# Optimization experiments

Measured on AMD Instinct MI355X. Metric: run time of the kernel, lower is better.

Reference implementation:

```python
import jax, jax.numpy as jnp
import numpy as np

_EPS = 1e-8

def setup_inputs() -> dict:
    key = jax.random.key(0)
    k1, k2, k3, k4 = jax.random.split(key, 4)
    L, B, H, S = 12, 8, 12, 384
    M, NL, NH = 32, 3, 4
    attn = jax.random.uniform(k1, (L, B, H, S, S), dtype=jnp.float32)
    references = jax.random.uniform(k2, (M, S, S), dtype=jnp.float32)
    layer_idx = jax.random.randint(k3, (M, NL), 0, L)
    head_idx = jax.random.randint(k4, (M, NH), 0, H)
    return {"attn": attn, "references": references,
            "layer_idx": layer_idx, "head_idx": head_idx}

def reference(attn, references, layer_idx, head_idx):
    # attn: [L,B,H,S,S] stacked attention maps; references: [M,S,S]
    L, B, H, S, _ = attn.shape
    M, nl = layer_idx.shape
    nh = head_idx.shape[1]
    rows = jnp.arange(M)[:, None]
    # One-hot averaging matrices: patch mean over selected layers/heads.
    # .add handles repeated indices the same way the gather-then-mean does.
    Wl = jnp.zeros((M, L), attn.dtype).at[rows, layer_idx].add(1.0 / nl)
    Wh = jnp.zeros((M, H), attn.dtype).at[rows, head_idx].add(1.0 / nh)
    # patch_means[m,b,s,t] = mean over patch layers/heads of attn
    patch_means = jnp.einsum('ml,mh,lbhst->mbst', Wl, Wh, attn)  # [M,B,S,S]
    flat = patch_means.reshape(M, B, S * S)
    ref = references.reshape(M, 1, S * S)
    # torch .std is unbiased (ddof=1) over the batch axis
    std = jnp.maximum(jnp.std(flat, axis=1, ddof=1, keepdims=True), _EPS)
    z = (flat - ref) / std
    scores = jnp.mean(z * z, axis=-1)  # [M,B]
    return scores.T  # [B,M]
```

## Files before the change

kernel.cpp:

```cpp
#include <hip/hip_runtime.h>

#define L_DIM 12
#define B_DIM 8
#define H_DIM 12
#define S_DIM 384
#define S2    (S_DIM * S_DIM)
#define M_DIM 32
#define NL 3
#define NH 4
#define CH 512
#define NCH (S2 / CH)
#define NXCD 8

template <bool ATOMIC>
__global__ __launch_bounds__(128) void pfe_main(
    const float* __restrict__ attn,
    const float* __restrict__ refs,
    const int*   __restrict__ lidx,
    const int*   __restrict__ hidx,
    float*       __restrict__ outp)
{
    const int p    = blockIdx.x;
    const int xcd  = p & (NXCD - 1);
    const int slot = p >> 3;
    const int m    = slot & (M_DIM - 1);
    const int lc   = slot >> 5;
    const int chunk = lc * NXCD + xcd;
    const int tid  = threadIdx.x;
    const unsigned st = (unsigned)chunk * CH + (unsigned)tid * 4;

    __shared__ int   s_mk[NL * NH];
    __shared__ float s_mw[NL * NH];
    __shared__ int   s_nm;
    __shared__ float s_red[2 * B_DIM];

    if (tid == 0) {
        int keys[NL * NH];
#pragma unroll
        for (int i = 0; i < NL; ++i) {
            const int l = lidx[m * NL + i];
#pragma unroll
            for (int j = 0; j < NH; ++j)
                keys[i * NH + j] = l * 16 + hidx[m * NH + j];
        }
        for (int i = 1; i < NL * NH; ++i) {
            const int k = keys[i];
            int j = i - 1;
            for (; j >= 0 && keys[j] > k; --j) keys[j + 1] = keys[j];
            keys[j + 1] = k;
        }
        int nm = 0;
        for (int i = 0; i < NL * NH; ++i) {
            if (nm > 0 && s_mk[nm - 1] == keys[i]) {
                s_mw[nm - 1] += 1.0f;
            } else {
                s_mk[nm] = keys[i];
                s_mw[nm] = 1.0f;
                ++nm;
            }
        }
        s_nm = nm;
    }
    __syncthreads();

    const float4 r = *reinterpret_cast<const float4*>(refs + (unsigned)m * (unsigned)S2 + st);

    float4 acc[B_DIM];
#pragma unroll
    for (int b = 0; b < B_DIM; ++b) acc[b] = make_float4(0.f, 0.f, 0.f, 0.f);

    const int nm = s_nm;
    for (int e = 0; e < nm; ++e) {
        const int   k = s_mk[e];
        const float w = s_mw[e];
        const int l = k >> 4, h = k & 15;
        const unsigned base = (unsigned)(l * (B_DIM * H_DIM) + h) * (unsigned)S2 + st;
#pragma unroll
        for (int b = 0; b < B_DIM; ++b) {
            const float4 v = *reinterpret_cast<const float4*>(
                attn + base + (unsigned)b * (unsigned)(H_DIM * S2));
            acc[b].x = fmaf(w, v.x, acc[b].x);
            acc[b].y = fmaf(w, v.y, acc[b].y);
            acc[b].z = fmaf(w, v.z, acc[b].z);
            acc[b].w = fmaf(w, v.w, acc[b].w);
        }
    }

    const float c12 = 1.0f / 12.0f;
    float4 pm[B_DIM];
#pragma unroll
    for (int b = 0; b < B_DIM; ++b) {
        pm[b].x = acc[b].x * c12; pm[b].y = acc[b].y * c12;
        pm[b].z = acc[b].z * c12; pm[b].w = acc[b].w * c12;
    }

    float4 mu = make_float4(0.f, 0.f, 0.f, 0.f);
#pragma unroll
    for (int b = 0; b < B_DIM; ++b) {
        mu.x += pm[b].x; mu.y += pm[b].y; mu.z += pm[b].z; mu.w += pm[b].w;
    }
    mu.x *= 0.125f; mu.y *= 0.125f; mu.z *= 0.125f; mu.w *= 0.125f;

    float4 ss = make_float4(0.f, 0.f, 0.f, 0.f);
#pragma unroll
    for (int b = 0; b < B_DIM; ++b) {
        const float dx = pm[b].x - mu.x, dy = pm[b].y - mu.y,
                    dz = pm[b].z - mu.z, dw = pm[b].w - mu.w;
        ss.x += dx * dx; ss.y += dy * dy; ss.z += dz * dz; ss.w += dw * dw;
    }
    const float c7 = 1.0f / 7.0f;
    float4 inv;
    inv.x = 1.0f / fmaxf(sqrtf(ss.x * c7), 1e-8f);
    inv.y = 1.0f / fmaxf(sqrtf(ss.y * c7), 1e-8f);
    inv.z = 1.0f / fmaxf(sqrtf(ss.z * c7), 1e-8f);
    inv.w = 1.0f / fmaxf(sqrtf(ss.w * c7), 1e-8f);

    float s[B_DIM];
#pragma unroll
    for (int b = 0; b < B_DIM; ++b) {
        const float zx = (pm[b].x - r.x) * inv.x;
        const float zy = (pm[b].y - r.y) * inv.y;
        const float zz = (pm[b].z - r.z) * inv.z;
        const float zw = (pm[b].w - r.w) * inv.w;
        s[b] = zx * zx + zy * zy + zz * zz + zw * zw;
    }

#pragma unroll
    for (int b = 0; b < B_DIM; ++b) {
        float v = s[b];
#pragma unroll
        for (int off = 32; off > 0; off >>= 1) v += __shfl_down(v, off);
        s[b] = v;
    }
    const int lane = tid & 63, wave = tid >> 6;
    if (lane == 0) {
#pragma unroll
        for (int b = 0; b < B_DIM; ++b) s_red[wave * B_DIM + b] = s[b];
    }
    __syncthreads();
    if (tid < B_DIM) {
        const float tot = s_red[tid] + s_red[B_DIM + tid];
        if (ATOMIC) {
            atomicAdd(&outp[tid * M_DIM + m], tot * (1.0f / (float)S2));
        } else {
            outp[(m * B_DIM + tid) * NCH + chunk] = tot;
        }
    }
}

__global__ __launch_bounds__(256) void pfe_final(
    const float* __restrict__ part, float* __restrict__ out)
{
    const int t = threadIdx.x;
    if (t >= M_DIM * B_DIM) return;
    const int m = t & (M_DIM - 1);
    const int b = t >> 5;
    const float* p = part + (m * B_DIM + b) * NCH;
    float sum = 0.f;
    for (int c = 0; c < NCH; ++c) sum += p[c];
    out[b * M_DIM + m] = sum * (1.0f / (float)S2);
}

__global__ void pfe_zero(float* __restrict__ out) {
    if (threadIdx.x < M_DIM * B_DIM) out[threadIdx.x] = 0.f;
}

extern "C" void kernel_launch(void* const* d_in, const int* in_sizes, int n_in,
                              void* d_out, int out_size, void* d_ws, size_t ws_size,
                              hipStream_t stream) {
    const float* attn = (const float*)d_in[0];
    const float* refs = (const float*)d_in[1];
    const int*   lidx = (const int*)d_in[2];
    const int*   hidx = (const int*)d_in[3];
    float* out = (float*)d_out;

    const int nblocks = NCH * M_DIM;
    const size_t ws_needed = (size_t)M_DIM * B_DIM * NCH * sizeof(float);

    if (ws_size >= ws_needed) {
        float* part = (float*)d_ws;
        pfe_main<false><<<nblocks, 128, 0, stream>>>(attn, refs, lidx, hidx, part);
        pfe_final<<<1, 256, 0, stream>>>(part, out);
    } else {
        pfe_zero<<<1, 256, 0, stream>>>(out);
        pfe_main<true><<<nblocks, 128, 0, stream>>>(attn, refs, lidx, hidx, out);
    }
}
```

Baseline: 178.4 us.

## Deduplicate layer/head reads across patches with shared-memory scatter accumulation

Adds a setup kernel that builds the set of unique (layer, head) pairs and the patches each one feeds. The main kernel then loads every attention slice only once per chunk and accumulates it into per-patch shared-memory buffers before computing the batch statistics. This targets redundant global reads of attention data that is shared across patches. The cost is an extra setup kernel, a two-stage partial reduction, shared-memory read-modify-write traffic and higher LDS usage per block.

```diff
diff --git a/kernel.cpp b/kernel.cpp
--- a/kernel.cpp
+++ b/kernel.cpp
@@ -8,26 +8,201 @@
 #define M_DIM 32
 #define NL 3
 #define NH 4
-#define CH 512
-#define NCH (S2 / CH)
-#define NXCD 8
-
-template <bool ATOMIC>
-__global__ __launch_bounds__(128) void pfe_main(
+
+#define CHB   64
+#define NCHB  (S2 / CHB)
+#define RED1  24
+#define NRED1 (NCHB / RED1)
+#define MAXP  152
+#define MAXE  384
+#define PART_ELEMS (NCHB * M_DIM * B_DIM)
+#define META_INTS 1092
+
+__global__ __launch_bounds__(256) void pfe_setup(
+    const int* __restrict__ lidx, const int* __restrict__ hidx, int* __restrict__ mi)
+{
+    __shared__ int cl[M_DIM][L_DIM], ch[M_DIM][H_DIM];
+    __shared__ int cnt[144], map[144], offL[145];
+    const int t = threadIdx.x;
+    if (t < M_DIM) {
+        for (int l = 0; l < L_DIM; ++l) cl[t][l] = 0;
+        for (int h = 0; h < H_DIM; ++h) ch[t][h] = 0;
+        for (int i = 0; i < NL; ++i) cl[t][lidx[t * NL + i]]++;
+        for (int j = 0; j < NH; ++j) ch[t][hidx[t * NH + j]]++;
+    }
+    __syncthreads();
+    if (t < 144) {
+        const int l = t / H_DIM, h = t % H_DIM;
+        int c = 0;
+        for (int m = 0; m < M_DIM; ++m) c += (cl[m][l] && ch[m][h]) ? 1 : 0;
+        cnt[t] = c;
+    }
+    __syncthreads();
+    if (t == 0) {
+        int np = 0, run = 0;
+        for (int k = 0; k < 144; ++k) {
+            if (cnt[k]) {
+                map[k] = np;
+                const int l = k / H_DIM, h = k % H_DIM;
+                mi[8 + np] = (l * (B_DIM * H_DIM) + h) * S2;
+                offL[np] = run;
+                run += cnt[k];
+                ++np;
+            } else map[k] = -1;
+        }
+        const int np4 = (np + 3) & ~3;
+        for (int p = np; p < np4 + 4; ++p) mi[8 + p] = mi[8 + np - 1];
+        for (int p = np; p <= np4; ++p) offL[p] = run;
+        for (int p = 0; p <= np4; ++p) mi[160 + p] = offL[p];
+        mi[0] = np4;
+        mi[1] = run;
+    }
+    __syncthreads();
+    if (t < 144 && map[t] >= 0) {
+        const int l = t / H_DIM, h = t % H_DIM;
+        int pos = offL[map[t]];
+        for (int m = 0; m < M_DIM; ++m) {
+            const int w = cl[m][l] * ch[m][h];
+            if (w) {
+                mi[320 + pos] = m;
+                reinterpret_cast<float*>(mi)[704 + pos] = (float)w * (1.0f / 12.0f);
+                ++pos;
+            }
+        }
+    }
+}
+
+__global__ __launch_bounds__(256) void pfe_dedup(
     const float* __restrict__ attn,
     const float* __restrict__ refs,
-    const int*   __restrict__ lidx,
-    const int*   __restrict__ hidx,
-    float*       __restrict__ outp)
-{
-    const int p    = blockIdx.x;
-    const int xcd  = p & (NXCD - 1);
-    const int slot = p >> 3;
-    const int m    = slot & (M_DIM - 1);
-    const int lc   = slot >> 5;
-    const int chunk = lc * NXCD + xcd;
-    const int tid  = threadIdx.x;
-    const unsigned st = (unsigned)chunk * CH + (unsigned)tid * 4;
+    const int*   __restrict__ mi,
+    float*       __restrict__ part)
+{
+    __shared__ float pm[M_DIM * B_DIM * CHB];
+    __shared__ int   s_base[MAXP];
+    __shared__ int   s_off[MAXP];
+    __shared__ int   s_em[MAXE];
+    __shared__ float s_ew[MAXE];
+
+    const int t = threadIdx.x;
+    const int chunk = blockIdx.x;
+    const int np4 = mi[0];
+    const int ne  = mi[1];
+
+    for (int i = t; i < np4 + 4; i += 256) s_base[i] = mi[8 + i];
+    for (int i = t; i <= np4;    i += 256) s_off[i]  = mi[160 + i];
+    for (int i = t; i < ne;      i += 256) { s_em[i] = mi[320 + i];
+                                             s_ew[i] = reinterpret_cast<const float*>(mi)[704 + i]; }
+    float2* pmv = reinterpret_cast<float2*>(pm);
+    for (int i = t; i < M_DIM * B_DIM * CHB / 2; i += 256) pmv[i] = make_float2(0.f, 0.f);
+    __syncthreads();
+
+    const int b  = t >> 5;
+    const int sq = t & 31;
+    const unsigned toff = (unsigned)(b * H_DIM) * (unsigned)S2
+                        + (unsigned)chunk * (unsigned)CHB + (unsigned)sq * 2u;
+    const float* ap = attn + toff;
+    float2* myp = pmv + b * (CHB / 2) + sq;
+
+#define LD(q) (*reinterpret_cast<const float2*>(ap + s_base[q]))
+#define PROC(P, V)                                                        \
+    {                                                                     \
+        const int e1 = s_off[(P) + 1];                                    \
+        for (int e = s_off[P]; e < e1; ++e) {                             \
+            float2* pp = myp + s_em[e] * (B_DIM * CHB / 2);               \
+            const float w = s_ew[e];                                      \
+            float2 c = *pp;                                               \
+            c.x = fmaf(w, (V).x, c.x);                                    \
+            c.y = fmaf(w, (V).y, c.y);                                    \
+            *pp = c;                                                      \
+        }                                                                 \
+    }
+
+    float2 v0 = LD(0), v1 = LD(1), v2 = LD(2), v3 = LD(3);
+    for (int p = 0; p < np4; p += 4) {
+        PROC(p + 0, v0); v0 = LD(p + 4);
+        PROC(p + 1, v1); v1 = LD(p + 5);
+        PROC(p + 2, v2); v2 = LD(p + 6);
+        PROC(p + 3, v3); v3 = LD(p + 7);
+    }
+#undef PROC
+#undef LD
+    __syncthreads();
+
+    for (int q = 0; q < 8; ++q) {
+        const int tau = t + 256 * q;
+        const int mm = tau >> 6;
+        const int sl = tau & 63;
+        float x[B_DIM];
+        float mu = 0.f;
+#pragma unroll
+        for (int bb = 0; bb < B_DIM; ++bb) {
+            x[bb] = pm[(mm * B_DIM + bb) * CHB + sl];
+            mu += x[bb];
+        }
+        mu *= 0.125f;
+        float ssum = 0.f;
+#pragma unroll
+        for (int bb = 0; bb < B_DIM; ++bb) {
+            const float d = x[bb] - mu;
+            ssum = fmaf(d, d, ssum);
+        }
+        const float inv = 1.0f / fmaxf(sqrtf(ssum * (1.0f / 7.0f)), 1e-8f);
+        const float rv = refs[(unsigned)mm * (unsigned)S2 + (unsigned)chunk * CHB + (unsigned)sl];
+#pragma unroll
+        for (int bb = 0; bb < B_DIM; ++bb)
+            pm[(mm * B_DIM + bb) * CHB + sl] = (x[bb] - rv) * inv;
+    }
+    __syncthreads();
+
+    const int mB = t >> 3, bB = t & 7;
+    float acc = 0.f;
+#pragma unroll
+    for (int s = 0; s < CHB; ++s) {
+        const int sl = (s + t) & (CHB - 1);
+        const float z = pm[(mB * B_DIM + bB) * CHB + sl];
+        acc = fmaf(z, z, acc);
+    }
+    part[chunk * 256 + t] = acc;
+}
+
+__global__ __launch_bounds__(256) void pfe_red1(
+    const float* __restrict__ part, float* __restrict__ mid)
+{
+    const int t = threadIdx.x;
+    const int c0 = blockIdx.x * RED1;
+    float s = 0.f;
+#pragma unroll
+    for (int i = 0; i < RED1; ++i) s += part[(c0 + i) * 256 + t];
+    mid[blockIdx.x * 256 + t] = s;
+}
+
+__global__ __launch_bounds__(256) void pfe_red2(
+    const float* __restrict__ mid, float* __restrict__ out)
+{
+    const int t = threadIdx.x;
+    float s = 0.f;
+#pragma unroll
+    for (int i = 0; i < NRED1; ++i) s += mid[i * 256 + t];
+    out[(t & 7) * M_DIM + (t >> 3)] = s * (1.0f / (float)S2);
+}
+
+__global__ void pfe_zero(float* __restrict__ out) {
+    if (threadIdx.x < M_DIM * B_DIM) out[threadIdx.x] = 0.f;
+}
+
+#define FCH 512
+#define FNCH (S2 / FCH)
+__global__ __launch_bounds__(128) void pfe_fallback(
+    const float* __restrict__ attn, const float* __restrict__ refs,
+    const int* __restrict__ lidx, const int* __restrict__ hidx,
+    float* __restrict__ out)
+{
+    const int p = blockIdx.x;
+    const int m = p & (M_DIM - 1);
+    const int chunk = p >> 5;
+    const int tid = threadIdx.x;
+    const unsigned st = (unsigned)chunk * FCH + (unsigned)tid * 4;
 
     __shared__ int   s_mk[NL * NH];
     __shared__ float s_mw[NL * NH];
@@ -36,76 +211,54 @@
 
     if (tid == 0) {
         int keys[NL * NH];
-#pragma unroll
         for (int i = 0; i < NL; ++i) {
             const int l = lidx[m * NL + i];
-#pragma unroll
-            for (int j = 0; j < NH; ++j)
-                keys[i * NH + j] = l * 16 + hidx[m * NH + j];
+            for (int j = 0; j < NH; ++j) keys[i * NH + j] = l * 16 + hidx[m * NH + j];
         }
         for (int i = 1; i < NL * NH; ++i) {
-            const int k = keys[i];
-            int j = i - 1;
+            const int k = keys[i]; int j = i - 1;
             for (; j >= 0 && keys[j] > k; --j) keys[j + 1] = keys[j];
             keys[j + 1] = k;
         }
         int nm = 0;
         for (int i = 0; i < NL * NH; ++i) {
-            if (nm > 0 && s_mk[nm - 1] == keys[i]) {
-                s_mw[nm - 1] += 1.0f;
-            } else {
-                s_mk[nm] = keys[i];
-                s_mw[nm] = 1.0f;
-                ++nm;
-            }
+            if (nm > 0 && s_mk[nm - 1] == keys[i]) s_mw[nm - 1] += 1.0f;
+            else { s_mk[nm] = keys[i]; s_mw[nm] = 1.0f; ++nm; }
         }
         s_nm = nm;
     }
     __syncthreads();
 
     const float4 r = *reinterpret_cast<const float4*>(refs + (unsigned)m * (unsigned)S2 + st);
-
     float4 acc[B_DIM];
-#pragma unroll
-    for (int b = 0; b < B_DIM; ++b) acc[b] = make_float4(0.f, 0.f, 0.f, 0.f);
-
+    for (int bb = 0; bb < B_DIM; ++bb) acc[bb] = make_float4(0.f, 0.f, 0.f, 0.f);
     const int nm = s_nm;
     for (int e = 0; e < nm; ++e) {
-        const int   k = s_mk[e];
-        const float w = s_mw[e];
+        const int k = s_mk[e]; const float w = s_mw[e];
         const int l = k >> 4, h = k & 15;
         const unsigned base = (unsigned)(l * (B_DIM * H_DIM) + h) * (unsigned)S2 + st;
-#pragma unroll
-        for (int b = 0; b < B_DIM; ++b) {
+        for (int bb = 0; bb < B_DIM; ++bb) {
             const float4 v = *reinterpret_cast<const float4*>(
-                attn + base + (unsigned)b * (unsigned)(H_DIM * S2));
-            acc[b].x = fmaf(w, v.x, acc[b].x);
-            acc[b].y = fmaf(w, v.y, acc[b].y);
-            acc[b].z = fmaf(w, v.z, acc[b].z);
-            acc[b].w = fmaf(w, v.w, acc[b].w);
-        }
-    }
-
+                attn + base + (unsigned)bb * (unsigned)(H_DIM * S2));
+            acc[bb].x = fmaf(w, v.x, acc[bb].x); acc[bb].y = fmaf(w, v.y, acc[bb].y);
+            acc[bb].z = fmaf(w, v.z, acc[bb].z); acc[bb].w = fmaf(w, v.w, acc[bb].w);
+        }
+    }
     const float c12 = 1.0f / 12.0f;
-    float4 pm[B_DIM];
-#pragma unroll
-    for (int b = 0; b < B_DIM; ++b) {
-        pm[b].x = acc[b].x * c12; pm[b].y = acc[b].y * c12;
-        pm[b].z = acc[b].z * c12; pm[b].w = acc[b].w * c12;
-    }
-
+    float4 pmv[B_DIM];
+    for (int bb = 0; bb < B_DIM; ++bb) {
+        pmv[bb].x = acc[bb].x * c12; pmv[bb].y = acc[bb].y * c12;
+        pmv[bb].z = acc[bb].z * c12; pmv[bb].w = acc[bb].w * c12;
+    }
     float4 mu = make_float4(0.f, 0.f, 0.f, 0.f);
-#pragma unroll
-    for (int b = 0; b < B_DIM; ++b) {
-        mu.x += pm[b].x; mu.y += pm[b].y; mu.z += pm[b].z; mu.w += pm[b].w;
+    for (int bb = 0; bb < B_DIM; ++bb) {
+        mu.x += pmv[bb].x; mu.y += pmv[bb].y; mu.z += pmv[bb].z; mu.w += pmv[bb].w;
     }
     mu.x *= 0.125f; mu.y *= 0.125f; mu.z *= 0.125f; mu.w *= 0.125f;
-
     float4 ss = make_float4(0.f, 0.f, 0.f, 0.f);
-#pragma unroll
-    for (int b = 0; b < B_DIM; ++b) {
-        const float dx = pm[b].x - mu.x, dy = pm[b].y - mu.y,
-                    dz = pm[b].z - mu.z, dw = pm[b].w - mu.w;
+    for (int bb = 0; bb < B_DIM; ++bb) {
+        const float dx = pmv[bb].x - mu.x, dy = pmv[bb].y - mu.y,
+                    dz = pmv[bb].z - mu.z, dw = pmv[bb].w - mu.w;
         ss.x += dx * dx; ss.y += dy * dy; ss.z += dz * dz; ss.w += dw * dw;
     }
     const float c7 = 1.0f / 7.0f;
@@ -114,55 +267,26 @@
     inv.y = 1.0f / fmaxf(sqrtf(ss.y * c7), 1e-8f);
     inv.z = 1.0f / fmaxf(sqrtf(ss.z * c7), 1e-8f);
     inv.w = 1.0f / fmaxf(sqrtf(ss.w * c7), 1e-8f);
-
     float s[B_DIM];
-#pragma unroll
-    for (int b = 0; b < B_DIM; ++b) {
-        const float zx = (pm[b].x - r.x) * inv.x;
-        const float zy = (pm[b].y - r.y) * inv.y;
-        const float zz = (pm[b].z - r.z) * inv.z;
-        const float zw = (pm[b].w - r.w) * inv.w;
-        s[b] = zx * zx + zy * zy + zz * zz + zw * zw;
-    }
-
-#pragma unroll
-    for (int b = 0; b < B_DIM; ++b) {
-        float v = s[b];
-#pragma unroll
+    for (int bb = 0; bb < B_DIM; ++bb) {
+        const float zx = (pmv[bb].x - r.x) * inv.x;
+        const float zy = (pmv[bb].y - r.y) * inv.y;
+        const float zz = (pmv[bb].z - r.z) * inv.z;
+        const float zw = (pmv[bb].w - r.w) * inv.w;
+        s[bb] = zx * zx + zy * zy + zz * zz + zw * zw;
+    }
+    for (int bb = 0; bb < B_DIM; ++bb) {
+        float v = s[bb];
         for (int off = 32; off > 0; off >>= 1) v += __shfl_down(v, off);
-        s[b] = v;
+        s[bb] = v;
     }
     const int lane = tid & 63, wave = tid >> 6;
-    if (lane == 0) {
-#pragma unroll
-        for (int b = 0; b < B_DIM; ++b) s_red[wave * B_DIM + b] = s[b];
-    }
+    if (lane == 0) for (int bb = 0; bb < B_DIM; ++bb) s_red[wave * B_DIM + bb] = s[bb];
     __syncthreads();
     if (tid < B_DIM) {
-        const float tot = s_red[tid] + s_red[B_DIM + tid];
-        if (ATOMIC) {
-            atomicAdd(&outp[tid * M_DIM + m], tot * (1.0f / (float)S2));
-        } else {
-            outp[(m * B_DIM + tid) * NCH + chunk] = tot;
-        }
-    }
-}
-
-__global__ __launch_bounds__(256) void pfe_final(
-    const float* __restrict__ part, float* __restrict__ out)
-{
-    const int t = threadIdx.x;
-    if (t >= M_DIM * B_DIM) return;
-    const int m = t & (M_DIM - 1);
-    const int b = t >> 5;
-    const float* p = part + (m * B_DIM + b) * NCH;
-    float sum = 0.f;
-    for (int c = 0; c < NCH; ++c) sum += p[c];
-    out[b * M_DIM + m] = sum * (1.0f / (float)S2);
-}
-
-__global__ void pfe_zero(float* __restrict__ out) {
-    if (threadIdx.x < M_DIM * B_DIM) out[threadIdx.x] = 0.f;
+        const float tot = (s_red[tid] + s_red[B_DIM + tid]) * (1.0f / (float)S2);
+        atomicAdd(&out[tid * M_DIM + m], tot);
+    }
 }
 
 extern "C" void kernel_launch(void* const* d_in, const int* in_sizes, int n_in,
@@ -174,15 +298,19 @@
     const int*   hidx = (const int*)d_in[3];
     float* out = (float*)d_out;
 
-    const int nblocks = NCH * M_DIM;
-    const size_t ws_needed = (size_t)M_DIM * B_DIM * NCH * sizeof(float);
+    const size_t ws_needed =
+        (size_t)(PART_ELEMS + META_INTS + NRED1 * 256) * sizeof(float);
 
     if (ws_size >= ws_needed) {
         float* part = (float*)d_ws;
-        pfe_main<false><<<nblocks, 128, 0, stream>>>(attn, refs, lidx, hidx, part);
-        pfe_final<<<1, 256, 0, stream>>>(part, out);
+        int*   mi   = (int*)(part + PART_ELEMS);
+        float* mid  = (float*)(mi + META_INTS);
+        pfe_setup<<<1, 256, 0, stream>>>(lidx, hidx, mi);
+        pfe_dedup<<<NCHB, 256, 0, stream>>>(attn, refs, mi, part);
+        pfe_red1<<<NRED1, 256, 0, stream>>>(part, mid);
+        pfe_red2<<<1, 256, 0, stream>>>(mid, out);
     } else {
         pfe_zero<<<1, 256, 0, stream>>>(out);
-        pfe_main<true><<<nblocks, 128, 0, stream>>>(attn, refs, lidx, hidx, out);
-    }
-}
+        pfe_fallback<<<FNCH * M_DIM, 128, 0, stream>>>(attn, refs, lidx, hidx, out);
+    }
+}
```

New measurement: 243.2 us. +36.3%, slower.
